# Optimization experiments

Measured on AMD Instinct MI355X. Metric: run time of the kernel, lower is better.

The kernel has to match this reference:

```python
import jax, jax.numpy as jnp
import numpy as np

K = 20            # neighbors
C = 21            # num_classes
P = 16            # patch_size
NROWS = 14        # img_size // patch_size
H = NROWS * P     # 224
TEMP = 1.0        # temperature


def setup_inputs() -> dict:
    key = jax.random.key(0)
    k1, k2, k3 = jax.random.split(key, 3)
    test_feature = jax.random.normal(k1, (8, 196, 384), dtype=jnp.float32)
    train_features = jax.random.normal(k2, (384, 50000), dtype=jnp.float32)
    train_labels = jax.random.randint(k3, (256, 50000), 0, C, dtype=jnp.int32)
    return {"test_feature": test_feature, "train_features": train_features,
            "train_labels": train_labels}


def reference(test_feature, train_features, train_labels):
    bs = test_feature.shape[0]
    # similarity: [bs, num_patches, N_train]
    sim = jnp.einsum('bpd,dn->bpn', test_feature, train_features)
    sim_k, idx = jax.lax.top_k(sim, K)              # [bs, 196, K]
    # gather neighbor patch labels: train_labels [P^2, N] -> [bs, 196, K, P^2]
    nb = train_labels.T[idx]
    # make_grid with nrow=NROWS, padding=0: assemble patches into [bs, K, H, H]
    nb = nb.reshape(bs, NROWS, NROWS, K, P, P)
    nb = nb.transpose(0, 3, 1, 4, 2, 5).reshape(bs, K, H, H)
    nb = nb.transpose(0, 2, 3, 1)                   # [bs, H, H, K]
    # weighted majority vote: nearest-upsample similarities 14x14 -> 224x224
    w = sim_k.reshape(bs, NROWS, NROWS, K)
    w = jnp.repeat(jnp.repeat(w, P, axis=1), P, axis=2)   # [bs, H, H, K]
    w = jax.nn.softmax(w / TEMP, axis=-1)
    # one-hot vote expressed as scatter-add over classes (same math, no
    # [bs,H,H,K,C] materialization)
    rows = jnp.arange(bs * H * H)
    vote = jnp.zeros((bs * H * H, C), dtype=w.dtype)
    vote = vote.at[rows[:, None], nb.reshape(bs * H * H, K)].add(
        w.reshape(bs * H * H, K))
    vote = vote.reshape(bs, H, H, C)
    pred = jnp.argmax(vote, axis=-1)                # [bs, H, H] int
    return pred
```

## Files before the change

### kernel.cpp

```cpp
#include <hip/hip_runtime.h>
#include <float.h>

#define N_TRAIN 50000
#define NPAD    50176
#define NBLKS   392
#define MPAD    1664
#define DDIM    384
#define M_ROWS  1568
#define KNN     20
#define K2      24
#define SELMAX  64
#define NCLS    21
#define CAPBUF  768
#define NENT    1568

typedef __attribute__((ext_vector_type(8))) short bf16x8;
typedef __attribute__((ext_vector_type(4))) float f32x4;

#define GLOAD_LDS16(gp, lp) \
  __builtin_amdgcn_global_load_lds((const __attribute__((address_space(1))) void*)(gp), \
                                   (__attribute__((address_space(3))) void*)(lp), 16, 0, 0)

static __device__ __forceinline__ unsigned short f2bf(float f) {
  unsigned int u = __float_as_uint(f);
  unsigned int r = (u + 0x7fffu + ((u >> 16) & 1u)) >> 16;
  return (unsigned short)r;
}
static __device__ __forceinline__ float bf2f(unsigned short h) {
  return __uint_as_float(((unsigned int)h) << 16);
}
static __device__ __forceinline__ unsigned int flip32(unsigned int u) {
  return (u & 0x80000000u) ? ~u : (u | 0x80000000u);
}

#define CSW(x, y) { unsigned int _hi = max(x, y); unsigned int _lo = min(x, y); x = _hi; y = _lo; }

__global__ __launch_bounds__(256) void transpose_labels(const int* __restrict__ labels,
                                                        unsigned char* __restrict__ labT) {
  __shared__ int tile[64][65];
  const int t  = threadIdx.x;
  const int c0 = blockIdx.x * 64;
  const int r0 = blockIdx.y * 64;
#pragma unroll
  for (int i = 0; i < 16; ++i) {
    int idx = i * 256 + t;
    int r = idx >> 6, c = idx & 63;
    int cc = c0 + c;
    tile[r][c] = (cc < N_TRAIN) ? labels[(size_t)(r0 + r) * N_TRAIN + cc] : 0;
  }
  __syncthreads();
#pragma unroll
  for (int i = 0; i < 16; ++i) {
    int idx = i * 256 + t;
    int c = idx >> 6, r = idx & 63;
    int cc = c0 + c;
    if (cc < N_TRAIN) labT[(size_t)cc * 256 + r0 + r] = (unsigned char)tile[r][c];
  }
}

__global__ __launch_bounds__(256) void conv_Apack(const float* __restrict__ test,
                                                  unsigned short* __restrict__ Apack) {
  int o = blockIdx.x * 256 + threadIdx.x;
  if (o >= (MPAD / 16) * 12 * 512) return;
  int j = o & 7;
  int l = (o >> 3) & 63;
  int kcmt = o >> 9;
  int kc = kcmt % 12, mt = kcmt / 12;
  int row = mt * 16 + (l & 15);
  int k = kc * 32 + (l >> 4) * 8 + j;
  Apack[o] = (row < M_ROWS) ? f2bf(test[(size_t)row * DDIM + k]) : (unsigned short)0;
}

__global__ __launch_bounds__(256) void trans_train_fused(const float* __restrict__ train,
                                                         unsigned short* __restrict__ Bpack,
                                                         float* __restrict__ trainT) {
  __shared__ float tile[64][65];
  const int t  = threadIdx.x;
  const int c0 = blockIdx.x * 64;
  const int r0 = blockIdx.y * 64;
#pragma unroll
  for (int i = 0; i < 16; ++i) {
    int idx = i * 256 + t;
    int r = idx >> 6, c = idx & 63;
    int cc = c0 + c;
    tile[r][c] = (cc < N_TRAIN) ? train[(size_t)(r0 + r) * N_TRAIN + cc] : 0.f;
  }
  __syncthreads();
#pragma unroll
  for (int it = 0; it < 2; ++it) {
    int u = it * 256 + t;
    int c = u & 63, koctL = u >> 6;
    int col = c0 + c;
    int koct = (r0 >> 3) + koctL;
    int kc = koct >> 2, l4 = koct & 3;
    int nt = col >> 4, l15 = col & 15;
    size_t base = ((size_t)(nt * 12 + kc) * 64 + l4 * 16 + l15) * 8;
    ushort4 h0, h1;
    h0.x = f2bf(tile[koctL * 8 + 0][c]); h0.y = f2bf(tile[koctL * 8 + 1][c]);
    h0.z = f2bf(tile[koctL * 8 + 2][c]); h0.w = f2bf(tile[koctL * 8 + 3][c]);
    h1.x = f2bf(tile[koctL * 8 + 4][c]); h1.y = f2bf(tile[koctL * 8 + 5][c]);
    h1.z = f2bf(tile[koctL * 8 + 6][c]); h1.w = f2bf(tile[koctL * 8 + 7][c]);
    *(ushort4*)&Bpack[base]     = h0;
    *(ushort4*)&Bpack[base + 4] = h1;
  }
#pragma unroll
  for (int i = 0; i < 16; ++i) {
    int idx = i * 256 + t;
    int c = idx >> 6, r = idx & 63;
    int cc = c0 + c;
    if (cc < N_TRAIN) trainT[(size_t)cc * DDIM + r0 + r] = tile[r][c];
  }
}

__global__ __launch_bounds__(512, 2) void mfma_gemm(const unsigned short* __restrict__ Apack,
                                                    const unsigned short* __restrict__ Bpack,
                                                    unsigned int* __restrict__ toplist) {
  extern __shared__ unsigned short lds16[];
  uint4* bounce = (uint4*)((char*)lds16 + 98304);
  const int t = threadIdx.x;

  const int flat = blockIdx.x;
  const int xcd = flat & 7, jj = flat >> 3;
  const int wg = (xcd < 5 ? xcd * 80 : 400 + (xcd - 5) * 79) + jj;
  const int mblk = wg % 13, ngrp = wg / 13;
  const int m0 = mblk * 128;

  const int wid = t >> 6, lane = t & 63;
  const int wr = wid >> 2, wc = wid & 3;
  const int l15 = lane & 15, l4 = lane >> 4;

  const unsigned short* Asrc = Apack + (size_t)(mblk * 8) * 12 * 512;
#pragma unroll
  for (int j = 0; j < 12; ++j)
    GLOAD_LDS16(Asrc + (size_t)j * 4096 + wid * 512 + lane * 8,
                &lds16[j * 4096 + wid * 512]);
  __syncthreads();

#pragma unroll 1
  for (int s = 0; s < 2; ++s) {
    const int colbase = ngrp * 1024 + s * 512;
    const unsigned short* Bb = Bpack + (size_t)(colbase / 16 + wc * 8) * 12 * 512;

    f32x4 acc[4][8];
    const f32x4 zero = {0.f, 0.f, 0.f, 0.f};
#pragma unroll
    for (int f = 0; f < 4; ++f)
#pragma unroll
      for (int n = 0; n < 8; ++n) acc[f][n] = zero;

#pragma unroll 2
    for (int kc = 0; kc < 12; ++kc) {
      bf16x8 a[4], b[8];
#pragma unroll
      for (int n = 0; n < 8; ++n)
        b[n] = *(const bf16x8*)&Bb[((size_t)(n * 12 + kc) * 64 + lane) * 8];
#pragma unroll
      for (int f = 0; f < 4; ++f)
        a[f] = *(const bf16x8*)&lds16[((wr * 4 + f) * 12 + kc) * 512 + lane * 8];
#pragma unroll
      for (int f = 0; f < 4; ++f)
#pragma unroll
        for (int n = 0; n < 8; ++n)
          acc[f][n] = __builtin_amdgcn_mfma_f32_16x16x32_bf16(a[f], b[n], acc[f][n], 0, 0, 0);
    }

#pragma unroll
    for (int f = 0; f < 4; ++f) {
#pragma unroll
      for (int r = 0; r < 4; ++r) {
        unsigned int e[8];
#pragma unroll
        for (int n = 0; n < 8; ++n) {
          int col = colbase + wc * 128 + n * 16 + l15;
          unsigned int k16 = flip32(__float_as_uint(acc[f][n][r])) >> 16;
          e[n] = (col < N_TRAIN) ? ((k16 << 16) | (0xFFFFu - (unsigned int)col)) : 0u;
        }
        CSW(e[0], e[1]); CSW(e[2], e[3]); CSW(e[0], e[2]); CSW(e[1], e[3]); CSW(e[1], e[2]);
        CSW(e[4], e[5]); CSW(e[6], e[7]); CSW(e[4], e[6]); CSW(e[5], e[7]); CSW(e[5], e[6]);
        unsigned int v0 = max(e[0], e[7]), v1 = max(e[1], e[6]);
        unsigned int v2 = max(e[2], e[5]), v3 = max(e[3], e[4]);
        CSW(v0, v2); CSW(v1, v3); CSW(v0, v1); CSW(v2, v3);
#pragma unroll
        for (int st = 1; st <= 8; st <<= 1) {
          unsigned int p0 = (unsigned int)__shfl_xor((int)v0, st);
          unsigned int p1 = (unsigned int)__shfl_xor((int)v1, st);
          unsigned int p2 = (unsigned int)__shfl_xor((int)v2, st);
          unsigned int p3 = (unsigned int)__shfl_xor((int)v3, st);
          unsigned int t0 = max(v0, p3), t1 = max(v1, p2);
          unsigned int t2 = max(v2, p1), t3 = max(v3, p0);
          CSW(t0, t2); CSW(t1, t3); CSW(t0, t1); CSW(t2, t3);
          v0 = t0; v1 = t1; v2 = t2; v3 = t3;
        }
        if (l15 == 0) {
          uint4 w; w.x = v0; w.y = v1; w.z = v2; w.w = v3;
          bounce[(wr * 64 + f * 16 + l4 * 4 + r) * 4 + wc] = w;
        }
      }
    }
    __syncthreads();

    {
      int row = t >> 2, e = t & 3;
      int grow = m0 + row;
      if (grow < M_ROWS) {
        uint4 w = bounce[row * 4 + e];
        int blk = ngrp * 8 + s * 4 + e;
        *(uint4*)&toplist[(size_t)grow * NENT + blk * 4] = w;
      }
    }
    __syncthreads();
  }
}

__global__ __launch_bounds__(256) void tail_fused(const unsigned int* __restrict__ toplist,
                                                  const float* __restrict__ test,
                                                  const float* __restrict__ trainT,
                                                  const unsigned char* __restrict__ labT,
                                                  int* __restrict__ out) {
  const int t = threadIdx.x, m = blockIdx.x;
  __shared__ unsigned int ent[NENT];
  __shared__ unsigned int smax[256];
  __shared__ unsigned int sbuf[CAPBUF];
  __shared__ unsigned int scnt, sTauA, sE24, ccnt2;
  __shared__ unsigned char flg[NBLKS];
  __shared__ short flist[64];
  __shared__ int fcnt, sC2;
  __shared__ unsigned int cbuf[128];
  __shared__ int    selC[SELMAX];
  __shared__ double rvs[SELMAX];
  __shared__ double sv2[SELMAX];
  __shared__ int    si2[SELMAX];
  __shared__ double earr[KNN];
  __shared__ double wv[KNN];
  __shared__ int    wi[KNN];

  if (t == 0) { scnt = 0u; fcnt = 0; ccnt2 = 0u; sC2 = 0; }
  for (int i = t; i < NENT; i += 256) ent[i] = toplist[(size_t)m * NENT + i];
  __syncthreads();

  unsigned int mx = 0u;
  for (int i = t; i < NENT; i += 256) mx = max(mx, ent[i]);
  smax[t] = mx;
  __syncthreads();
  {
    int rnk = 0;
    for (int j = 0; j < 256; ++j)
      rnk += (smax[j] > mx || (smax[j] == mx && j < t)) ? 1 : 0;
    if (rnk == K2 - 1) sTauA = mx;
  }
  __syncthreads();
  const unsigned int tauA = sTauA;

  for (int i = t; i < NENT; i += 256) {
    unsigned int e = ent[i];
    if (e >= tauA) { unsigned int p = atomicAdd(&scnt, 1u); if (p < CAPBUF) sbuf[p] = e; }
  }
  __syncthreads();
  const int C = (int)min(scnt, (unsigned int)CAPBUF);
  for (int s = t; s < C; s += 256) {
    unsigned int e = sbuf[s];
    int rk = 0;
    for (int j = 0; j < C; ++j) rk += (sbuf[j] > e) ? 1 : 0;
    if (rk == K2 - 1) sE24 = e;
  }
  __syncthreads();
  const unsigned int k24 = sE24 >> 16;

  for (int i = t; i < NBLKS; i += 256) {
    bool fl = (ent[i * 4 + 3] >> 16) >= k24;
    flg[i] = fl ? 1 : 0;
    if (fl) { int p = atomicAdd(&fcnt, 1); if (p < 64) flist[p] = (short)i; }
  }
  __syncthreads();

  for (int i = t; i < NENT; i += 256) {
    unsigned int e = ent[i];
    if ((e >> 16) >= k24) {
      int col = 0xFFFF - (int)(e & 0xFFFFu);
      if (!flg[col >> 7]) { unsigned int p = atomicAdd(&ccnt2, 1u); if (p < 128) cbuf[p] = e; }
    }
  }
  __syncthreads();

  const int FC = min(fcnt, 64);
  for (int q = 0; q < FC; ++q) {
    const int fb = flist[q];
    const int col = fb * 128 + t;
    if (t < 128 && col < N_TRAIN) {
      const float* Tc = trainT + (size_t)col * DDIM;
      const float* Tr = test + (size_t)m * DDIM;
      float s0 = 0.f;
      for (int k = 0; k < DDIM; ++k)
        s0 = fmaf(bf2f(f2bf(Tr[k])), bf2f(f2bf(Tc[k])), s0);
      unsigned int key = flip32(__float_as_uint(s0)) >> 16;
      if (key + 1u >= k24) {
        unsigned int e = (key << 16) | (0xFFFFu - (unsigned int)col);
        unsigned int p = atomicAdd(&ccnt2, 1u);
        if (p < 128) cbuf[p] = e;
      }
    }
  }
  __syncthreads();
  const int CC = (int)min(ccnt2, 128u);

  for (int s = t; s < CC; s += 256) {
    unsigned int e = cbuf[s];
    int rk = 0;
    for (int j = 0; j < CC; ++j) rk += (cbuf[j] > e) ? 1 : 0;
    if (rk < SELMAX) {
      selC[rk] = 0xFFFF - (int)(e & 0xFFFFu);
      atomicMax(&sC2, rk + 1);
    }
  }
  __syncthreads();
  const int C2 = sC2 < SELMAX ? sC2 : SELMAX;

  const int wid = t >> 6, lane = t & 63;
  float tr[DDIM / 64];
#pragma unroll
  for (int dd = 0; dd < DDIM / 64; ++dd)
    tr[dd] = test[(size_t)m * DDIM + dd * 64 + lane];
#pragma unroll 1
  for (int c = wid; c < C2; c += 4) {
    const float* Tc = trainT + (size_t)selC[c] * DDIM;
    double s = 0.0;
#pragma unroll
    for (int dd = 0; dd < DDIM / 64; ++dd)
      s += (double)tr[dd] * (double)Tc[dd * 64 + lane];
#pragma unroll
    for (int off = 32; off > 0; off >>= 1) s += __shfl_xor(s, off);
    if (lane == 0) rvs[c] = s;
  }
  __syncthreads();

  if (t < C2) {
    double v = rvs[t]; int id = selC[t];
    int r = 0;
    for (int n = 0; n < C2; ++n)
      r += (rvs[n] > v || (rvs[n] == v && selC[n] < id)) ? 1 : 0;
    sv2[r] = v; si2[r] = id;
  }
  __syncthreads();

  if (t < KNN) earr[t] = exp(sv2[t] - sv2[0]);
  __syncthreads();
  if (t < KNN) {
    double ssum = 0.0;
    for (int k = 0; k < KNN; ++k) ssum += earr[k];
    wv[t] = earr[t] / ssum;
    wi[t] = si2[t];
  }
  __syncthreads();

  unsigned int packed[5];
#pragma unroll
  for (int q = 0; q < 5; ++q) {
    unsigned int p = 0;
#pragma unroll
    for (int j = 0; j < 4; ++j)
      p |= (unsigned int)labT[(size_t)wi[q * 4 + j] * 256 + t] << (8 * j);
    packed[q] = p;
  }
  double best = -1.0; int bc = 0;
#pragma unroll 1
  for (int c = 0; c < NCLS; ++c) {
    double s = 0.0;
#pragma unroll
    for (int k = 0; k < KNN; ++k) {
      unsigned int lab = (packed[k >> 2] >> ((k & 3) * 8)) & 255u;
      s += (lab == (unsigned int)c) ? wv[k] : 0.0;
    }
    if (s > best) { best = s; bc = c; }
  }
  const int b = m / 196, p = m % 196;
  const int py = p / 14, px = p % 14;
  const int i = t >> 4, j = t & 15;
  out[((size_t)b * 224 + py * 16 + i) * 224 + px * 16 + j] = bc;
}

extern "C" void kernel_launch(void* const* d_in, const int* in_sizes, int n_in,
                              void* d_out, int out_size, void* d_ws, size_t ws_size,
                              hipStream_t stream) {
  const float* test  = (const float*)d_in[0];
  const float* train = (const float*)d_in[1];
  const int* labels  = (const int*)d_in[2];
  int* out = (int*)d_out;
  char* ws = (char*)d_ws;

  unsigned char*  labT    = (unsigned char*)ws;
  unsigned short* Apack   = (unsigned short*)(ws + 12800000);
  unsigned short* Bpack   = (unsigned short*)(ws + 14077952);
  float*          trainT  = (float*)(ws + 52613120);
  unsigned int*   toplist = (unsigned int*)(ws + 129413120);

  transpose_labels<<<dim3(782, 4), 256, 0, stream>>>(labels, labT);
  conv_Apack<<<dim3((MPAD / 16) * 12 * 512 / 256), 256, 0, stream>>>(test, Apack);
  trans_train_fused<<<dim3(784, 6), 256, 0, stream>>>(train, Bpack, trainT);
  mfma_gemm<<<dim3(637), 512, 106496, stream>>>(Apack, Bpack, toplist);
  tail_fused<<<dim3(M_ROWS), 256, 0, stream>>>(toplist, test, trainT, labT, out);
}
```

Before: 234.1 us.

## Switch GEMM to 32x32x16 MFMA with smaller M tiles and higher occupancy

Repacks the A and B operands for the 32x32x16 bf16 MFMA layout and rewrites the GEMM to use it. M blocks shrink from 128 to 64 rows, so the grid doubles, LDS use drops to static arrays, and launch bounds allow 4 blocks per CU. The per-row top-4 reduction is rebuilt around 32-lane groups. The aim is higher MFMA throughput per instruction and better latency hiding from more resident waves. In exchange, B traffic per output rises because M tiles are smaller, and register pressure under the tighter launch bound may force spills.

After: 243.6 us. 4.1% more time.

```diff
diff --git a/kernel.cpp b/kernel.cpp
--- a/kernel.cpp
+++ b/kernel.cpp
@@ -14,8 +14,8 @@
 #define CAPBUF  768
 #define NENT    1568
 
-typedef __attribute__((ext_vector_type(8))) short bf16x8;
-typedef __attribute__((ext_vector_type(4))) float f32x4;
+typedef __attribute__((ext_vector_type(8)))  short bf16x8;
+typedef __attribute__((ext_vector_type(16))) float f32x16;
 
 #define GLOAD_LDS16(gp, lp) \
   __builtin_amdgcn_global_load_lds((const __attribute__((address_space(1))) void*)(gp), \
@@ -61,13 +61,13 @@
 __global__ __launch_bounds__(256) void conv_Apack(const float* __restrict__ test,
                                                   unsigned short* __restrict__ Apack) {
   int o = blockIdx.x * 256 + threadIdx.x;
-  if (o >= (MPAD / 16) * 12 * 512) return;
+  if (o >= (MPAD / 32) * 24 * 512) return;
   int j = o & 7;
   int l = (o >> 3) & 63;
-  int kcmt = o >> 9;
-  int kc = kcmt % 12, mt = kcmt / 12;
-  int row = mt * 16 + (l & 15);
-  int k = kc * 32 + (l >> 4) * 8 + j;
+  int rest = o >> 9;
+  int ks = rest % 24, mt = rest / 24;
+  int row = mt * 32 + (l & 31);
+  int k = ks * 16 + (l >> 5) * 8 + j;
   Apack[o] = (row < M_ROWS) ? f2bf(test[(size_t)row * DDIM + k]) : (unsigned short)0;
 }
 
@@ -92,9 +92,9 @@
     int c = u & 63, koctL = u >> 6;
     int col = c0 + c;
     int koct = (r0 >> 3) + koctL;
-    int kc = koct >> 2, l4 = koct & 3;
-    int nt = col >> 4, l15 = col & 15;
-    size_t base = ((size_t)(nt * 12 + kc) * 64 + l4 * 16 + l15) * 8;
+    int ks = koct >> 1, half = koct & 1;
+    int nt = col >> 5, l = (c & 31) + half * 32;
+    size_t base = ((size_t)(nt * 24 + ks) * 64 + l) * 8;
     ushort4 h0, h1;
     h0.x = f2bf(tile[koctL * 8 + 0][c]); h0.y = f2bf(tile[koctL * 8 + 1][c]);
     h0.z = f2bf(tile[koctL * 8 + 2][c]); h0.w = f2bf(tile[koctL * 8 + 3][c]);
@@ -112,99 +112,92 @@
   }
 }
 
-__global__ __launch_bounds__(512, 2) void mfma_gemm(const unsigned short* __restrict__ Apack,
+__global__ __launch_bounds__(512, 4) void mfma_gemm(const unsigned short* __restrict__ Apack,
                                                     const unsigned short* __restrict__ Bpack,
                                                     unsigned int* __restrict__ toplist) {
-  extern __shared__ unsigned short lds16[];
-  uint4* bounce = (uint4*)((char*)lds16 + 98304);
+  __shared__ unsigned short Al[24576];
+  __shared__ uint4 bounce[64 * 4];
   const int t = threadIdx.x;
 
   const int flat = blockIdx.x;
   const int xcd = flat & 7, jj = flat >> 3;
-  const int wg = (xcd < 5 ? xcd * 80 : 400 + (xcd - 5) * 79) + jj;
-  const int mblk = wg % 13, ngrp = wg / 13;
-  const int m0 = mblk * 128;
+  const int wg = (xcd < 2 ? xcd * 160 : 320 + (xcd - 2) * 159) + jj;
+  const int mblk = wg % 26, ngrp = wg / 26;
+  const int m0 = mblk * 64;
 
   const int wid = t >> 6, lane = t & 63;
   const int wr = wid >> 2, wc = wid & 3;
-  const int l15 = lane & 15, l4 = lane >> 4;
-
-  const unsigned short* Asrc = Apack + (size_t)(mblk * 8) * 12 * 512;
-#pragma unroll
-  for (int j = 0; j < 12; ++j)
+  const int l31 = lane & 31, lh = lane >> 5;
+
+  const unsigned short* Asrc = Apack + (size_t)(mblk * 2) * 24 * 512;
+#pragma unroll
+  for (int j = 0; j < 6; ++j)
     GLOAD_LDS16(Asrc + (size_t)j * 4096 + wid * 512 + lane * 8,
-                &lds16[j * 4096 + wid * 512]);
+                &Al[j * 4096 + wid * 512]);
   __syncthreads();
 
 #pragma unroll 1
   for (int s = 0; s < 2; ++s) {
     const int colbase = ngrp * 1024 + s * 512;
-    const unsigned short* Bb = Bpack + (size_t)(colbase / 16 + wc * 8) * 12 * 512;
-
-    f32x4 acc[4][8];
-    const f32x4 zero = {0.f, 0.f, 0.f, 0.f};
-#pragma unroll
-    for (int f = 0; f < 4; ++f)
-#pragma unroll
-      for (int n = 0; n < 8; ++n) acc[f][n] = zero;
-
-#pragma unroll 2
-    for (int kc = 0; kc < 12; ++kc) {
-      bf16x8 a[4], b[8];
-#pragma unroll
-      for (int n = 0; n < 8; ++n)
-        b[n] = *(const bf16x8*)&Bb[((size_t)(n * 12 + kc) * 64 + lane) * 8];
-#pragma unroll
-      for (int f = 0; f < 4; ++f)
-        a[f] = *(const bf16x8*)&lds16[((wr * 4 + f) * 12 + kc) * 512 + lane * 8];
-#pragma unroll
-      for (int f = 0; f < 4; ++f)
-#pragma unroll
-        for (int n = 0; n < 8; ++n)
-          acc[f][n] = __builtin_amdgcn_mfma_f32_16x16x32_bf16(a[f], b[n], acc[f][n], 0, 0, 0);
-    }
-
-#pragma unroll
-    for (int f = 0; f < 4; ++f) {
-#pragma unroll
-      for (int r = 0; r < 4; ++r) {
-        unsigned int e[8];
-#pragma unroll
-        for (int n = 0; n < 8; ++n) {
-          int col = colbase + wc * 128 + n * 16 + l15;
-          unsigned int k16 = flip32(__float_as_uint(acc[f][n][r])) >> 16;
+    const unsigned short* Bb = Bpack + (size_t)((colbase >> 5) + wc * 4) * 24 * 512;
+
+    f32x16 acc[4];
+#pragma unroll
+    for (int n = 0; n < 4; ++n)
+#pragma unroll
+      for (int q = 0; q < 16; ++q) acc[n][q] = 0.f;
+
+#pragma unroll 4
+    for (int ks = 0; ks < 24; ++ks) {
+      bf16x8 a = *(const bf16x8*)&Al[((wr * 24 + ks) * 64 + lane) * 8];
+      bf16x8 b[4];
+#pragma unroll
+      for (int n = 0; n < 4; ++n)
+        b[n] = *(const bf16x8*)&Bb[((size_t)(n * 24 + ks) * 64 + lane) * 8];
+#pragma unroll
+      for (int n = 0; n < 4; ++n)
+        acc[n] = __builtin_amdgcn_mfma_f32_32x32x16_bf16(a, b[n], acc[n], 0, 0, 0);
+    }
+
+#pragma unroll
+    for (int reg = 0; reg < 16; ++reg) {
+      const int rowl = (reg & 3) + 8 * (reg >> 2) + 4 * lh;
+      unsigned int v0, v1, v2, v3;
+      {
+        unsigned int e[4];
+#pragma unroll
+        for (int n = 0; n < 4; ++n) {
+          int col = colbase + wc * 128 + n * 32 + l31;
+          unsigned int k16 = flip32(__float_as_uint(acc[n][reg])) >> 16;
           e[n] = (col < N_TRAIN) ? ((k16 << 16) | (0xFFFFu - (unsigned int)col)) : 0u;
         }
         CSW(e[0], e[1]); CSW(e[2], e[3]); CSW(e[0], e[2]); CSW(e[1], e[3]); CSW(e[1], e[2]);
-        CSW(e[4], e[5]); CSW(e[6], e[7]); CSW(e[4], e[6]); CSW(e[5], e[7]); CSW(e[5], e[6]);
-        unsigned int v0 = max(e[0], e[7]), v1 = max(e[1], e[6]);
-        unsigned int v2 = max(e[2], e[5]), v3 = max(e[3], e[4]);
-        CSW(v0, v2); CSW(v1, v3); CSW(v0, v1); CSW(v2, v3);
-#pragma unroll
-        for (int st = 1; st <= 8; st <<= 1) {
-          unsigned int p0 = (unsigned int)__shfl_xor((int)v0, st);
-          unsigned int p1 = (unsigned int)__shfl_xor((int)v1, st);
-          unsigned int p2 = (unsigned int)__shfl_xor((int)v2, st);
-          unsigned int p3 = (unsigned int)__shfl_xor((int)v3, st);
-          unsigned int t0 = max(v0, p3), t1 = max(v1, p2);
-          unsigned int t2 = max(v2, p1), t3 = max(v3, p0);
-          CSW(t0, t2); CSW(t1, t3); CSW(t0, t1); CSW(t2, t3);
-          v0 = t0; v1 = t1; v2 = t2; v3 = t3;
-        }
-        if (l15 == 0) {
-          uint4 w; w.x = v0; w.y = v1; w.z = v2; w.w = v3;
-          bounce[(wr * 64 + f * 16 + l4 * 4 + r) * 4 + wc] = w;
-        }
+        v0 = e[0]; v1 = e[1]; v2 = e[2]; v3 = e[3];
+      }
+#pragma unroll
+      for (int st = 1; st <= 16; st <<= 1) {
+        unsigned int p0 = (unsigned int)__shfl_xor((int)v0, st);
+        unsigned int p1 = (unsigned int)__shfl_xor((int)v1, st);
+        unsigned int p2 = (unsigned int)__shfl_xor((int)v2, st);
+        unsigned int p3 = (unsigned int)__shfl_xor((int)v3, st);
+        unsigned int t0 = max(v0, p3), t1 = max(v1, p2);
+        unsigned int t2 = max(v2, p1), t3 = max(v3, p0);
+        CSW(t0, t2); CSW(t1, t3); CSW(t0, t1); CSW(t2, t3);
+        v0 = t0; v1 = t1; v2 = t2; v3 = t3;
+      }
+      if (l31 == 0) {
+        uint4 w; w.x = v0; w.y = v1; w.z = v2; w.w = v3;
+        bounce[(wr * 32 + rowl) * 4 + wc] = w;
       }
     }
     __syncthreads();
 
-    {
+    if (t < 256) {
       int row = t >> 2, e = t & 3;
       int grow = m0 + row;
       if (grow < M_ROWS) {
         uint4 w = bounce[row * 4 + e];
-        int blk = ngrp * 8 + s * 4 + e;
+        int blk = (colbase >> 7) + e;
         *(uint4*)&toplist[(size_t)grow * NENT + blk * 4] = w;
       }
     }
@@ -394,8 +387,8 @@
   unsigned int*   toplist = (unsigned int*)(ws + 129413120);
 
   transpose_labels<<<dim3(782, 4), 256, 0, stream>>>(labels, labT);
-  conv_Apack<<<dim3((MPAD / 16) * 12 * 512 / 256), 256, 0, stream>>>(test, Apack);
+  conv_Apack<<<dim3((MPAD / 32) * 24 * 512 / 256), 256, 0, stream>>>(test, Apack);
   trans_train_fused<<<dim3(784, 6), 256, 0, stream>>>(train, Bpack, trainT);
-  mfma_gemm<<<dim3(637), 512, 106496, stream>>>(Apack, Bpack, toplist);
+  mfma_gemm<<<dim3(1274), 512, 0, stream>>>(Apack, Bpack, toplist);
   tail_fused<<<dim3(M_ROWS), 256, 0, stream>>>(toplist, test, trainT, labT, out);
 }
```

## Overlap GEMM with trainT/label transposes and halve GEMM M-tile

Applied to the files above, without the earlier changes.

Moves the fp32 trainT transpose and the label transpose into the same launch as the MFMA GEMM, as extra workgroups after the GEMM blocks, so the bandwidth-bound copies can run alongside compute-bound GEMM blocks. The Bpack and Apack packing kernels are merged into one prep launch. The GEMM M tile shrinks from 128 to 64 rows, which halves the LDS footprint and allows 4 blocks per CU, and s_setprio is raised around the MFMA loop. The smaller tile doubles B-operand reloads across the grid, and the mixed workgroups compete for the same CUs.

After: 242.0 us. 1.03x slower.

```diff
diff --git a/kernel.cpp b/kernel.cpp
--- a/kernel.cpp
+++ b/kernel.cpp
@@ -2,7 +2,6 @@
 #include <float.h>
 
 #define N_TRAIN 50000
-#define NPAD    50176
 #define NBLKS   392
 #define MPAD    1664
 #define DDIM    384
@@ -13,6 +12,9 @@
 #define NCLS    21
 #define CAPBUF  768
 #define NENT    1568
+#define NGEMM   1274
+#define NTRT    4704
+#define NLAB    3128
 
 typedef __attribute__((ext_vector_type(8))) short bf16x8;
 typedef __attribute__((ext_vector_type(4))) float f32x4;
@@ -35,103 +37,120 @@
 
 #define CSW(x, y) { unsigned int _hi = max(x, y); unsigned int _lo = min(x, y); x = _hi; y = _lo; }
 
-__global__ __launch_bounds__(256) void transpose_labels(const int* __restrict__ labels,
-                                                        unsigned char* __restrict__ labT) {
-  __shared__ int tile[64][65];
-  const int t  = threadIdx.x;
-  const int c0 = blockIdx.x * 64;
-  const int r0 = blockIdx.y * 64;
-#pragma unroll
-  for (int i = 0; i < 16; ++i) {
-    int idx = i * 256 + t;
-    int r = idx >> 6, c = idx & 63;
-    int cc = c0 + c;
-    tile[r][c] = (cc < N_TRAIN) ? labels[(size_t)(r0 + r) * N_TRAIN + cc] : 0;
-  }
-  __syncthreads();
-#pragma unroll
-  for (int i = 0; i < 16; ++i) {
-    int idx = i * 256 + t;
-    int c = idx >> 6, r = idx & 63;
-    int cc = c0 + c;
-    if (cc < N_TRAIN) labT[(size_t)cc * 256 + r0 + r] = (unsigned char)tile[r][c];
-  }
-}
-
-__global__ __launch_bounds__(256) void conv_Apack(const float* __restrict__ test,
-                                                  unsigned short* __restrict__ Apack) {
-  int o = blockIdx.x * 256 + threadIdx.x;
-  if (o >= (MPAD / 16) * 12 * 512) return;
-  int j = o & 7;
-  int l = (o >> 3) & 63;
-  int kcmt = o >> 9;
-  int kc = kcmt % 12, mt = kcmt / 12;
-  int row = mt * 16 + (l & 15);
-  int k = kc * 32 + (l >> 4) * 8 + j;
-  Apack[o] = (row < M_ROWS) ? f2bf(test[(size_t)row * DDIM + k]) : (unsigned short)0;
-}
-
-__global__ __launch_bounds__(256) void trans_train_fused(const float* __restrict__ train,
-                                                         unsigned short* __restrict__ Bpack,
-                                                         float* __restrict__ trainT) {
+__global__ __launch_bounds__(256) void prep_ab(const float* __restrict__ train,
+                                               const float* __restrict__ test,
+                                               unsigned short* __restrict__ Bpack,
+                                               unsigned short* __restrict__ Apack) {
   __shared__ float tile[64][65];
-  const int t  = threadIdx.x;
-  const int c0 = blockIdx.x * 64;
-  const int r0 = blockIdx.y * 64;
-#pragma unroll
-  for (int i = 0; i < 16; ++i) {
-    int idx = i * 256 + t;
-    int r = idx >> 6, c = idx & 63;
-    int cc = c0 + c;
-    tile[r][c] = (cc < N_TRAIN) ? train[(size_t)(r0 + r) * N_TRAIN + cc] : 0.f;
-  }
-  __syncthreads();
-#pragma unroll
-  for (int it = 0; it < 2; ++it) {
-    int u = it * 256 + t;
-    int c = u & 63, koctL = u >> 6;
-    int col = c0 + c;
-    int koct = (r0 >> 3) + koctL;
-    int kc = koct >> 2, l4 = koct & 3;
-    int nt = col >> 4, l15 = col & 15;
-    size_t base = ((size_t)(nt * 12 + kc) * 64 + l4 * 16 + l15) * 8;
-    ushort4 h0, h1;
-    h0.x = f2bf(tile[koctL * 8 + 0][c]); h0.y = f2bf(tile[koctL * 8 + 1][c]);
-    h0.z = f2bf(tile[koctL * 8 + 2][c]); h0.w = f2bf(tile[koctL * 8 + 3][c]);
-    h1.x = f2bf(tile[koctL * 8 + 4][c]); h1.y = f2bf(tile[koctL * 8 + 5][c]);
-    h1.z = f2bf(tile[koctL * 8 + 6][c]); h1.w = f2bf(tile[koctL * 8 + 7][c]);
-    *(ushort4*)&Bpack[base]     = h0;
-    *(ushort4*)&Bpack[base + 4] = h1;
-  }
-#pragma unroll
-  for (int i = 0; i < 16; ++i) {
-    int idx = i * 256 + t;
-    int c = idx >> 6, r = idx & 63;
-    int cc = c0 + c;
-    if (cc < N_TRAIN) trainT[(size_t)cc * DDIM + r0 + r] = tile[r][c];
-  }
-}
-
-__global__ __launch_bounds__(512, 2) void mfma_gemm(const unsigned short* __restrict__ Apack,
-                                                    const unsigned short* __restrict__ Bpack,
-                                                    unsigned int* __restrict__ toplist) {
+  const int b = blockIdx.x, t = threadIdx.x;
+
+  if (b < 4704) {
+    const int c0 = (b % 784) * 64;
+    const int r0 = (b / 784) * 64;
+#pragma unroll
+    for (int i = 0; i < 16; ++i) {
+      int idx = i * 256 + t;
+      int r = idx >> 6, c = idx & 63;
+      int cc = c0 + c;
+      tile[r][c] = (cc < N_TRAIN) ? train[(size_t)(r0 + r) * N_TRAIN + cc] : 0.f;
+    }
+    __syncthreads();
+#pragma unroll
+    for (int it = 0; it < 2; ++it) {
+      int u = it * 256 + t;
+      int c = u & 63, koctL = u >> 6;
+      int col = c0 + c;
+      int koct = (r0 >> 3) + koctL;
+      int kc = koct >> 2, l4 = koct & 3;
+      int nt = col >> 4, l15 = col & 15;
+      size_t base = ((size_t)(nt * 12 + kc) * 64 + l4 * 16 + l15) * 8;
+      ushort4 h0, h1;
+      h0.x = f2bf(tile[koctL * 8 + 0][c]); h0.y = f2bf(tile[koctL * 8 + 1][c]);
+      h0.z = f2bf(tile[koctL * 8 + 2][c]); h0.w = f2bf(tile[koctL * 8 + 3][c]);
+      h1.x = f2bf(tile[koctL * 8 + 4][c]); h1.y = f2bf(tile[koctL * 8 + 5][c]);
+      h1.z = f2bf(tile[koctL * 8 + 6][c]); h1.w = f2bf(tile[koctL * 8 + 7][c]);
+      *(ushort4*)&Bpack[base]     = h0;
+      *(ushort4*)&Bpack[base + 4] = h1;
+    }
+  } else {
+    int o = (b - 4704) * 256 + t;
+    int j = o & 7;
+    int l = (o >> 3) & 63;
+    int kcmt = o >> 9;
+    int kc = kcmt % 12, mt = kcmt / 12;
+    int row = mt * 16 + (l & 15);
+    int k = kc * 32 + (l >> 4) * 8 + j;
+    Apack[o] = (row < M_ROWS) ? f2bf(test[(size_t)row * DDIM + k]) : (unsigned short)0;
+  }
+}
+
+__global__ __launch_bounds__(512, 4) void fused_main(const unsigned short* __restrict__ Apack,
+                                                     const unsigned short* __restrict__ Bpack,
+                                                     const float* __restrict__ train,
+                                                     const int* __restrict__ labels,
+                                                     unsigned int* __restrict__ toplist,
+                                                     float* __restrict__ trainT,
+                                                     unsigned char* __restrict__ labT) {
   extern __shared__ unsigned short lds16[];
-  uint4* bounce = (uint4*)((char*)lds16 + 98304);
-  const int t = threadIdx.x;
-
-  const int flat = blockIdx.x;
-  const int xcd = flat & 7, jj = flat >> 3;
-  const int wg = (xcd < 5 ? xcd * 80 : 400 + (xcd - 5) * 79) + jj;
-  const int mblk = wg % 13, ngrp = wg / 13;
-  const int m0 = mblk * 128;
+  const int b = blockIdx.x, t = threadIdx.x;
+
+  if (b >= NGEMM) {
+    if (b < NGEMM + NTRT) {
+      float* ftile = (float*)lds16;
+      const int i2 = b - NGEMM;
+      const int c0 = (i2 % 784) * 64, r0 = (i2 / 784) * 64;
+#pragma unroll
+      for (int i = 0; i < 8; ++i) {
+        int idx = i * 512 + t;
+        int r = idx >> 6, c = idx & 63;
+        int cc = c0 + c;
+        ftile[r * 65 + c] = (cc < N_TRAIN) ? train[(size_t)(r0 + r) * N_TRAIN + cc] : 0.f;
+      }
+      __syncthreads();
+#pragma unroll
+      for (int i = 0; i < 8; ++i) {
+        int idx = i * 512 + t;
+        int c = idx >> 6, r = idx & 63;
+        int cc = c0 + c;
+        if (cc < N_TRAIN) trainT[(size_t)cc * DDIM + r0 + r] = ftile[r * 65 + c];
+      }
+    } else {
+      unsigned int* itile = (unsigned int*)lds16;
+      const int i3 = b - NGEMM - NTRT;
+      const int c0 = (i3 % 782) * 64, r0 = (i3 / 782) * 64;
+#pragma unroll
+      for (int i = 0; i < 8; ++i) {
+        int idx = i * 512 + t;
+        int r = idx >> 6, c = idx & 63;
+        int cc = c0 + c;
+        itile[r * 65 + c] = (cc < N_TRAIN) ? (unsigned int)labels[(size_t)(r0 + r) * N_TRAIN + cc] : 0u;
+      }
+      __syncthreads();
+#pragma unroll
+      for (int i = 0; i < 8; ++i) {
+        int idx = i * 512 + t;
+        int c = idx >> 6, r = idx & 63;
+        int cc = c0 + c;
+        if (cc < N_TRAIN) labT[(size_t)cc * 256 + r0 + r] = (unsigned char)itile[r * 65 + c];
+      }
+    }
+    return;
+  }
+
+  uint4* bounce = (uint4*)((char*)lds16 + 49152);
+
+  const int xcd = b & 7, jj = b >> 3;
+  const int wg = (xcd < 2 ? xcd * 160 : 320 + (xcd - 2) * 159) + jj;
+  const int mblk = wg % 26, ngrp = wg / 26;
+  const int m0 = mblk * 64;
 
   const int wid = t >> 6, lane = t & 63;
   const int wr = wid >> 2, wc = wid & 3;
   const int l15 = lane & 15, l4 = lane >> 4;
 
-  const unsigned short* Asrc = Apack + (size_t)(mblk * 8) * 12 * 512;
-#pragma unroll
-  for (int j = 0; j < 12; ++j)
+  const unsigned short* Asrc = Apack + (size_t)(mblk * 4) * 12 * 512;
+#pragma unroll
+  for (int j = 0; j < 6; ++j)
     GLOAD_LDS16(Asrc + (size_t)j * 4096 + wid * 512 + lane * 8,
                 &lds16[j * 4096 + wid * 512]);
   __syncthreads();
@@ -141,31 +160,33 @@
     const int colbase = ngrp * 1024 + s * 512;
     const unsigned short* Bb = Bpack + (size_t)(colbase / 16 + wc * 8) * 12 * 512;
 
-    f32x4 acc[4][8];
+    f32x4 acc[2][8];
     const f32x4 zero = {0.f, 0.f, 0.f, 0.f};
 #pragma unroll
-    for (int f = 0; f < 4; ++f)
+    for (int f = 0; f < 2; ++f)
 #pragma unroll
       for (int n = 0; n < 8; ++n) acc[f][n] = zero;
 
 #pragma unroll 2
     for (int kc = 0; kc < 12; ++kc) {
-      bf16x8 a[4], b[8];
+      bf16x8 a[2], bv[8];
 #pragma unroll
       for (int n = 0; n < 8; ++n)
-        b[n] = *(const bf16x8*)&Bb[((size_t)(n * 12 + kc) * 64 + lane) * 8];
-#pragma unroll
-      for (int f = 0; f < 4; ++f)
-        a[f] = *(const bf16x8*)&lds16[((wr * 4 + f) * 12 + kc) * 512 + lane * 8];
-#pragma unroll
-      for (int f = 0; f < 4; ++f)
+        bv[n] = *(const bf16x8*)&Bb[((size_t)(n * 12 + kc) * 64 + lane) * 8];
+#pragma unroll
+      for (int f = 0; f < 2; ++f)
+        a[f] = *(const bf16x8*)&lds16[((wr * 2 + f) * 12 + kc) * 512 + lane * 8];
+      __builtin_amdgcn_s_setprio(1);
+#pragma unroll
+      for (int f = 0; f < 2; ++f)
 #pragma unroll
         for (int n = 0; n < 8; ++n)
-          acc[f][n] = __builtin_amdgcn_mfma_f32_16x16x32_bf16(a[f], b[n], acc[f][n], 0, 0, 0);
-    }
-
-#pragma unroll
-    for (int f = 0; f < 4; ++f) {
+          acc[f][n] = __builtin_amdgcn_mfma_f32_16x16x32_bf16(a[f], bv[n], acc[f][n], 0, 0, 0);
+      __builtin_amdgcn_s_setprio(0);
+    }
+
+#pragma unroll
+    for (int f = 0; f < 2; ++f) {
 #pragma unroll
       for (int r = 0; r < 4; ++r) {
         unsigned int e[8];
@@ -193,13 +214,13 @@
         }
         if (l15 == 0) {
           uint4 w; w.x = v0; w.y = v1; w.z = v2; w.w = v3;
-          bounce[(wr * 64 + f * 16 + l4 * 4 + r) * 4 + wc] = w;
+          bounce[(wr * 32 + f * 16 + l4 * 4 + r) * 4 + wc] = w;
         }
       }
     }
     __syncthreads();
 
-    {
+    if (t < 256) {
       int row = t >> 2, e = t & 3;
       int grow = m0 + row;
       if (grow < M_ROWS) {
@@ -393,9 +414,8 @@
   float*          trainT  = (float*)(ws + 52613120);
   unsigned int*   toplist = (unsigned int*)(ws + 129413120);
 
-  transpose_labels<<<dim3(782, 4), 256, 0, stream>>>(labels, labT);
-  conv_Apack<<<dim3((MPAD / 16) * 12 * 512 / 256), 256, 0, stream>>>(test, Apack);
-  trans_train_fused<<<dim3(784, 6), 256, 0, stream>>>(train, Bpack, trainT);
-  mfma_gemm<<<dim3(637), 512, 106496, stream>>>(Apack, Bpack, toplist);
+  prep_ab<<<dim3(7200), 256, 0, stream>>>(train, test, Bpack, Apack);
+  fused_main<<<dim3(NGEMM + NTRT + NLAB), 512, 53248, stream>>>(
+      Apack, Bpack, train, labels, toplist, trainT, labT);
   tail_fused<<<dim3(M_ROWS), 256, 0, stream>>>(toplist, test, trainT, labT, out);
 }
```
